# Kernel optimization log

Hardware: AMD Instinct MI355X
Metric: run time of the kernel (lower is better)

The kernel has to match this reference:

```python
import jax, jax.numpy as jnp
import numpy as np

NUM_CLASS = 5
IN_SIZE = 4
OBS_LEN = 20
EMBED = 256
B = 2048
N = 64
NUM_MODES = 20
IN_DIM = IN_SIZE * OBS_LEN  # 80


def setup_inputs() -> dict:
    key = jax.random.key(0)
    ks = jax.random.split(key, 12)
    s = 1.0 / np.sqrt(IN_DIM)
    inp = {
        "obs": jax.random.normal(ks[0], (B, OBS_LEN, IN_SIZE), jnp.float32),
        "neis": jax.random.normal(ks[1], (B, N, OBS_LEN, IN_SIZE), jnp.float32),
        "self_labels": jax.random.randint(ks[2], (B,), 0, NUM_CLASS),
        "nei_labels": jax.random.randint(ks[3], (B, N), 0, NUM_CLASS + 1),
        "modes": jax.random.normal(ks[4], (NUM_CLASS, NUM_MODES, EMBED), jnp.float32),
        # per-class obs embedding (ModuleList of Linear(in_dim, embed))
        "obs_W": jax.random.uniform(ks[5], (NUM_CLASS, IN_DIM, EMBED), jnp.float32, -s, s),
        "obs_b": jax.random.uniform(ks[6], (NUM_CLASS, EMBED), jnp.float32, -s, s),
        # per-class neighbor embedding (num_class+1 Linears)
        "nei_W": jax.random.uniform(ks[7], (NUM_CLASS + 1, IN_DIM, EMBED), jnp.float32, -s, s),
        "nei_b": jax.random.uniform(ks[8], (NUM_CLASS + 1, EMBED), jnp.float32, -s, s),
        # mode embedding Linear(2*embed, embed)
        "mode_W": jax.random.uniform(ks[9], (2 * EMBED, EMBED), jnp.float32, -1.0 / np.sqrt(2 * EMBED), 1.0 / np.sqrt(2 * EMBED)),
        "mode_b": jax.random.uniform(ks[10], (EMBED,), jnp.float32, -1.0 / np.sqrt(2 * EMBED), 1.0 / np.sqrt(2 * EMBED)),
    }
    return inp


def reference(obs, neis, self_labels, nei_labels, modes, obs_W, obs_b, nei_W, nei_b, mode_W, mode_b):
    obs_f = obs.reshape(B, IN_DIM)            # [B, in_dim]
    neis_f = neis.reshape(B, N, IN_DIM)       # [B, N, in_dim]
    eps = jnp.float32(1e-4)

    # label-routed obs embedding: one-hot selects the per-class Linear
    oh_s = jax.nn.one_hot(self_labels, NUM_CLASS, dtype=obs.dtype)          # [B, C]
    x = jnp.einsum("bi,cio,bc->bo", obs_f, obs_W, oh_s) + obs_b[self_labels]  # [B, E]

    # elementwise reciprocal transform (class-independent, applied to every neighbor row)
    r = jnp.where(neis_f >= 0, 1.0 / (neis_f + eps), 1.0 / (neis_f - eps))   # [B, N, in_dim]

    # label-routed neighbor embedding over num_class+1 experts
    oh_n = jax.nn.one_hot(nei_labels, NUM_CLASS + 1, dtype=obs.dtype)        # [B, N, C+1]
    nei_feats = jnp.einsum("bni,cio,bnc->bno", r, nei_W, oh_n) + nei_b[nei_labels]  # [B, N, E]

    mode_feats = modes[self_labels]                                          # [B, M, E]
    x_tiled = jnp.broadcast_to(x[:, None, :], (B, NUM_MODES, EMBED))
    cat = jnp.concatenate([x_tiled, mode_feats], axis=-1)                    # [B, M, 2E]
    out = jnp.einsum("bmk,ko->bmo", cat, mode_W) + mode_b                    # [B, M, E]
    return (out, nei_feats)
```

## Files before the change

kernel.cpp:

```cpp
#include <hip/hip_runtime.h>

#define BATCH 2048
#define NNEI 64
#define IN_DIM 80
#define EMBED 256
#define NCLS 5
#define NMODES 20
#define NROWS (BATCH * NNEI)
#define NEXP (NCLS + 1)
#define BPC2 256
#define TM 16

typedef __attribute__((ext_vector_type(8))) short bf16x8;
typedef __attribute__((ext_vector_type(4))) float f32x4;
typedef __attribute__((ext_vector_type(4))) int i32x4;

__device__ inline unsigned short bf16_rne(float f) {
    unsigned u = __builtin_bit_cast(unsigned, f);
    unsigned r = (u + 0x7fffu + ((u >> 16) & 1u)) >> 16;
    return (unsigned short)r;
}
__device__ inline float bf16_to_f(unsigned short h) {
    unsigned u = ((unsigned)h) << 16;
    return __builtin_bit_cast(float, u);
}

__global__ void count_labels(const int* __restrict__ nei_labels, int* __restrict__ counts) {
    __shared__ int lc[NEXP];
    int t = threadIdx.x;
    if (t < NEXP) lc[t] = 0;
    __syncthreads();
    atomicAdd(&lc[nei_labels[blockIdx.x * 256 + t]], 1);
    __syncthreads();
    if (t < NEXP) atomicAdd(&counts[t], lc[t]);
}

__global__ void scan_offsets(const int* __restrict__ counts,
                             int* __restrict__ offsets, int* __restrict__ cursors) {
    int s = 0;
    for (int c = 0; c < NEXP; ++c) { offsets[c] = s; cursors[c] = s; s += counts[c]; }
}

__global__ void place_rows(const int* __restrict__ nei_labels,
                           int* __restrict__ cursors, int* __restrict__ rowids) {
    __shared__ int lc[NEXP], lb[NEXP];
    int t = threadIdx.x;
    if (t < NEXP) lc[t] = 0;
    __syncthreads();
    int r = blockIdx.x * 256 + t;
    int c = nei_labels[r];
    int lpos = atomicAdd(&lc[c], 1);
    __syncthreads();
    if (t < NEXP) lb[t] = atomicAdd(&cursors[t], lc[t]);
    __syncthreads();
    rowids[lb[c] + lpos] = r;
}

__global__ void wfrag_prep(const float* __restrict__ nei_W, unsigned short* __restrict__ wfrag) {
    int e = blockIdx.x;
    int l = threadIdx.x;
    int part = e & 1;
    int cfg = (e >> 1) & 15;
    int ks = (e >> 5) % 3;
    int c = e / 96;
    int col = cfg * 16 + (l & 15);
    unsigned short v[8] __attribute__((aligned(16)));
    #pragma unroll
    for (int j = 0; j < 8; ++j) {
        int k = ks * 32 + ((l >> 4) * 8) + j;
        float w = (k < IN_DIM) ? nei_W[((size_t)c * IN_DIM + k) * EMBED + col] : 0.f;
        unsigned short h = bf16_rne(w);
        if (part == 0) v[j] = h;
        else v[j] = bf16_rne(w - bf16_to_f(h));
    }
    unsigned short* dst = wfrag + ((size_t)e * 64 + l) * 8;
    *reinterpret_cast<i32x4*>(dst) = *reinterpret_cast<const i32x4*>(v);
}

__global__ void mode_proj(const float* __restrict__ modes,
                          const float* __restrict__ mode_W,
                          const float* __restrict__ mode_b,
                          float* __restrict__ proj) {
    int cm = blockIdx.x;
    int o = threadIdx.x;
    const float* mv = modes + (size_t)cm * EMBED;
    float acc = mode_b[o];
    #pragma unroll 8
    for (int k = 0; k < EMBED; ++k)
        acc = fmaf(mv[k], mode_W[(size_t)(EMBED + k) * EMBED + o], acc);
    proj[(size_t)cm * EMBED + o] = acc;
}

#define BPB 4
__global__ __launch_bounds__(256, 2)
void obs_mode(const float* __restrict__ obs, const int* __restrict__ self_labels,
              const float* __restrict__ obs_W, const float* __restrict__ obs_b,
              const float* __restrict__ mode_W, const float* __restrict__ proj,
              float* __restrict__ out0) {
    int b0 = blockIdx.x * BPB;
    int o = threadIdx.x;
    __shared__ float obs_s[BPB][IN_DIM];
    __shared__ float x_s[BPB][EMBED];
    __shared__ int cls_s[BPB];

    for (int t = threadIdx.x; t < BPB * IN_DIM; t += 256) {
        int bb = t / IN_DIM, k = t % IN_DIM;
        obs_s[bb][k] = obs[(size_t)(b0 + bb) * IN_DIM + k];
    }
    if (threadIdx.x < BPB) cls_s[threadIdx.x] = self_labels[b0 + threadIdx.x];
    __syncthreads();

    int c[BPB];
    float xacc[BPB];
    #pragma unroll
    for (int bb = 0; bb < BPB; ++bb) {
        c[bb] = cls_s[bb];
        xacc[bb] = obs_b[c[bb] * EMBED + o];
    }
    #pragma unroll 8
    for (int k = 0; k < IN_DIM; ++k) {
        #pragma unroll
        for (int bb = 0; bb < BPB; ++bb)
            xacc[bb] = fmaf(obs_s[bb][k],
                            obs_W[(size_t)c[bb] * IN_DIM * EMBED + (size_t)k * EMBED + o],
                            xacc[bb]);
    }
    #pragma unroll
    for (int bb = 0; bb < BPB; ++bb) x_s[bb][o] = xacc[bb];
    __syncthreads();

    float tacc[BPB] = {0.f, 0.f, 0.f, 0.f};
    #pragma unroll 8
    for (int k = 0; k < EMBED; ++k) {
        float wv = mode_W[(size_t)k * EMBED + o];
        #pragma unroll
        for (int bb = 0; bb < BPB; ++bb)
            tacc[bb] = fmaf(x_s[bb][k], wv, tacc[bb]);
    }
    #pragma unroll
    for (int bb = 0; bb < BPB; ++bb) {
        const float* pj = proj + (size_t)c[bb] * NMODES * EMBED;
        float* op = out0 + (size_t)(b0 + bb) * NMODES * EMBED;
        for (int m = 0; m < NMODES; ++m)
            op[m * EMBED + o] = tacc[bb] + pj[m * EMBED + o];
    }
}

__global__ __launch_bounds__(256)
void nei_gemv_mfma(const float* __restrict__ neis,
                   const unsigned short* __restrict__ wfrag,
                   const float* __restrict__ nei_b,
                   const int* __restrict__ counts, const int* __restrict__ offsets,
                   const int* __restrict__ rowids,
                   float* __restrict__ out_n) {
    const int c = blockIdx.x / BPC2;
    const int blk = blockIdx.x % BPC2;
    const int cnt = counts[c];
    const int ntiles = (cnt + TM - 1) / TM;
    if (blk >= ntiles) return;

    const int ch = threadIdx.x >> 6;
    const int l = threadIdx.x & 63;
    const int* mylist = rowids + offsets[c];

    bf16x8 wh[3][4], wl[3][4];
    {
        const unsigned short* wb = wfrag + (size_t)c * 96 * 64 * 8;
        #pragma unroll
        for (int ks = 0; ks < 3; ++ks)
            #pragma unroll
            for (int cf = 0; cf < 4; ++cf) {
                size_t base = ((((size_t)ks * 16 + (ch * 4 + cf)) * 2) * 64 + l) * 8;
                wh[ks][cf] = *reinterpret_cast<const bf16x8*>(wb + base);
                wl[ks][cf] = *reinterpret_cast<const bf16x8*>(wb + base + 64 * 8);
            }
    }
    float bias[4];
    #pragma unroll
    for (int cf = 0; cf < 4; ++cf)
        bias[cf] = nei_b[c * EMBED + (ch * 4 + cf) * 16 + (l & 15)];

    const int kc = (l >> 4) * 8;

    for (int tile = blk; tile < ntiles; tile += BPC2) {
        int gi = tile * TM + (l & 15);
        int rid = mylist[min(gi, cnt - 1)];
        const float* base = neis + (size_t)rid * IN_DIM;

        float f[24];
        #pragma unroll
        for (int ks = 0; ks < 3; ++ks) {
            int k0 = ks * 32 + kc;
            if (k0 + 8 > IN_DIM) k0 = 0;
            float4 x0 = *reinterpret_cast<const float4*>(base + k0);
            float4 x1 = *reinterpret_cast<const float4*>(base + k0 + 4);
            f[ks * 8 + 0] = x0.x; f[ks * 8 + 1] = x0.y; f[ks * 8 + 2] = x0.z; f[ks * 8 + 3] = x0.w;
            f[ks * 8 + 4] = x1.x; f[ks * 8 + 5] = x1.y; f[ks * 8 + 6] = x1.z; f[ks * 8 + 7] = x1.w;
        }

        bf16x8 ah[3], al[3];
        #pragma unroll
        for (int ks = 0; ks < 3; ++ks) {
            #pragma unroll
            for (int j = 0; j < 8; ++j) {
                float v = f[ks * 8 + j];
                float d = (v >= 0.f) ? (v + 1e-4f) : (v - 1e-4f);
                float r = __builtin_amdgcn_rcpf(d);
                unsigned short hi = bf16_rne(r);
                ah[ks][j] = (short)hi;
                al[ks][j] = (short)bf16_rne(r - bf16_to_f(hi));
            }
        }

        f32x4 acc[4];
        #pragma unroll
        for (int cf = 0; cf < 4; ++cf) acc[cf] = (f32x4){0.f, 0.f, 0.f, 0.f};
        #pragma unroll
        for (int ks = 0; ks < 3; ++ks) {
            #pragma unroll
            for (int cf = 0; cf < 4; ++cf) {
                acc[cf] = __builtin_amdgcn_mfma_f32_16x16x32_bf16(ah[ks], wh[ks][cf], acc[cf], 0, 0, 0);
                acc[cf] = __builtin_amdgcn_mfma_f32_16x16x32_bf16(al[ks], wh[ks][cf], acc[cf], 0, 0, 0);
                acc[cf] = __builtin_amdgcn_mfma_f32_16x16x32_bf16(ah[ks], wl[ks][cf], acc[cf], 0, 0, 0);
            }
        }

        int rb = (l >> 4) * 4;
        #pragma unroll
        for (int i = 0; i < 4; ++i) {
            int rid_i = __shfl(rid, rb + i);
            if (tile * TM + rb + i < cnt) {
                float* op = out_n + (size_t)rid_i * EMBED + (l & 15);
                #pragma unroll
                for (int cf = 0; cf < 4; ++cf)
                    op[(ch * 4 + cf) * 16] = acc[cf][i] + bias[cf];
            }
        }
    }
}

extern "C" void kernel_launch(void* const* d_in, const int* in_sizes, int n_in,
                              void* d_out, int out_size, void* d_ws, size_t ws_size,
                              hipStream_t stream) {
    const float* obs         = (const float*)d_in[0];
    const float* neis        = (const float*)d_in[1];
    const int*   self_labels = (const int*)d_in[2];
    const int*   nei_labels  = (const int*)d_in[3];
    const float* modes       = (const float*)d_in[4];
    const float* obs_W       = (const float*)d_in[5];
    const float* obs_b       = (const float*)d_in[6];
    const float* nei_W       = (const float*)d_in[7];
    const float* nei_b       = (const float*)d_in[8];
    const float* mode_W      = (const float*)d_in[9];
    const float* mode_b      = (const float*)d_in[10];

    float* out0  = (float*)d_out;
    float* out_n = out0 + (size_t)BATCH * NMODES * EMBED;

    char* ws = (char*)d_ws;
    int* counts  = (int*)ws;
    int* offsets = (int*)(ws + 64);
    int* cursors = (int*)(ws + 128);
    int* rowids  = (int*)(ws + 256);
    float* proj  = (float*)(ws + 256 + (size_t)NROWS * 4);
    unsigned short* wfrag = (unsigned short*)(ws + 256 + (size_t)NROWS * 4
                                              + (size_t)NCLS * NMODES * EMBED * 4);

    hipMemsetAsync(counts, 0, NEXP * sizeof(int), stream);

    count_labels<<<NROWS / 256, 256, 0, stream>>>(nei_labels, counts);
    scan_offsets<<<1, 1, 0, stream>>>(counts, offsets, cursors);
    place_rows<<<NROWS / 256, 256, 0, stream>>>(nei_labels, cursors, rowids);
    wfrag_prep<<<NEXP * 96, 64, 0, stream>>>(nei_W, wfrag);
    mode_proj<<<NCLS * NMODES, 256, 0, stream>>>(modes, mode_W, mode_b, proj);
    obs_mode<<<BATCH / BPB, 256, 0, stream>>>(obs, self_labels, obs_W, obs_b,
                                              mode_W, proj, out0);
    nei_gemv_mfma<<<NEXP * BPC2, 256, 0, stream>>>(neis, wfrag, nei_b,
                                                   counts, offsets, rowids, out_n);
}
```

Measured before the change: 113.7 us.

## Merge label binning into one pass, shrink grid and double-buffer neighbor tile loads

The separate count, scan and place kernels become a single binning kernel that writes row ids into per-class fixed-stride lists, which removes two launches. The neighbor MFMA kernel now runs on a 512-block grid split across the classes, with launch bounds allowing 2 blocks per unit. Its tile loop is software-pipelined with two register buffers so the next tile's global loads overlap the current tile's MFMA work. obs_mode processes 8 batch rows per block instead of 4. The costs are a much larger workspace for the per-class lists, higher register pressure from the double buffers, and fewer blocks per class.

After: 111.0 us. -2.4%, faster.

```diff
diff --git a/kernel.cpp b/kernel.cpp
--- a/kernel.cpp
+++ b/kernel.cpp
@@ -8,8 +8,8 @@
 #define NMODES 20
 #define NROWS (BATCH * NNEI)
 #define NEXP (NCLS + 1)
-#define BPC2 256
 #define TM 16
+#define GRID2 512
 
 typedef __attribute__((ext_vector_type(8))) short bf16x8;
 typedef __attribute__((ext_vector_type(4))) float f32x4;
@@ -25,24 +25,8 @@
     return __builtin_bit_cast(float, u);
 }
 
-__global__ void count_labels(const int* __restrict__ nei_labels, int* __restrict__ counts) {
-    __shared__ int lc[NEXP];
-    int t = threadIdx.x;
-    if (t < NEXP) lc[t] = 0;
-    __syncthreads();
-    atomicAdd(&lc[nei_labels[blockIdx.x * 256 + t]], 1);
-    __syncthreads();
-    if (t < NEXP) atomicAdd(&counts[t], lc[t]);
-}
-
-__global__ void scan_offsets(const int* __restrict__ counts,
-                             int* __restrict__ offsets, int* __restrict__ cursors) {
-    int s = 0;
-    for (int c = 0; c < NEXP; ++c) { offsets[c] = s; cursors[c] = s; s += counts[c]; }
-}
-
-__global__ void place_rows(const int* __restrict__ nei_labels,
-                           int* __restrict__ cursors, int* __restrict__ rowids) {
+__global__ void bin_rows(const int* __restrict__ nei_labels,
+                         int* __restrict__ counts, int* __restrict__ lists) {
     __shared__ int lc[NEXP], lb[NEXP];
     int t = threadIdx.x;
     if (t < NEXP) lc[t] = 0;
@@ -51,9 +35,9 @@
     int c = nei_labels[r];
     int lpos = atomicAdd(&lc[c], 1);
     __syncthreads();
-    if (t < NEXP) lb[t] = atomicAdd(&cursors[t], lc[t]);
-    __syncthreads();
-    rowids[lb[c] + lpos] = r;
+    if (t < NEXP) lb[t] = atomicAdd(&counts[t], lc[t]);
+    __syncthreads();
+    lists[(size_t)c * NROWS + lb[c] + lpos] = r;
 }
 
 __global__ void wfrag_prep(const float* __restrict__ nei_W, unsigned short* __restrict__ wfrag) {
@@ -91,7 +75,7 @@
     proj[(size_t)cm * EMBED + o] = acc;
 }
 
-#define BPB 4
+#define BPB 8
 __global__ __launch_bounds__(256, 2)
 void obs_mode(const float* __restrict__ obs, const int* __restrict__ self_labels,
               const float* __restrict__ obs_W, const float* __restrict__ obs_b,
@@ -117,7 +101,7 @@
         c[bb] = cls_s[bb];
         xacc[bb] = obs_b[c[bb] * EMBED + o];
     }
-    #pragma unroll 8
+    #pragma unroll 4
     for (int k = 0; k < IN_DIM; ++k) {
         #pragma unroll
         for (int bb = 0; bb < BPB; ++bb)
@@ -129,8 +113,10 @@
     for (int bb = 0; bb < BPB; ++bb) x_s[bb][o] = xacc[bb];
     __syncthreads();
 
-    float tacc[BPB] = {0.f, 0.f, 0.f, 0.f};
-    #pragma unroll 8
+    float tacc[BPB];
+    #pragma unroll
+    for (int bb = 0; bb < BPB; ++bb) tacc[bb] = 0.f;
+    #pragma unroll 4
     for (int k = 0; k < EMBED; ++k) {
         float wv = mode_W[(size_t)k * EMBED + o];
         #pragma unroll
@@ -146,22 +132,27 @@
     }
 }
 
-__global__ __launch_bounds__(256)
+__global__ __launch_bounds__(256, 2)
 void nei_gemv_mfma(const float* __restrict__ neis,
                    const unsigned short* __restrict__ wfrag,
                    const float* __restrict__ nei_b,
-                   const int* __restrict__ counts, const int* __restrict__ offsets,
-                   const int* __restrict__ rowids,
+                   const int* __restrict__ counts,
+                   const int* __restrict__ lists,
                    float* __restrict__ out_n) {
-    const int c = blockIdx.x / BPC2;
-    const int blk = blockIdx.x % BPC2;
+    const int b = blockIdx.x;
+    const int c = (b * NEXP) / GRID2;
+    const int cstart = (c * GRID2 + NEXP - 1) / NEXP;
+    const int cend = ((c + 1) * GRID2 + NEXP - 1) / NEXP;
+    const int blk = b - cstart;
+    const int nblk = cend - cstart;
     const int cnt = counts[c];
     const int ntiles = (cnt + TM - 1) / TM;
-    if (blk >= ntiles) return;
+    if (blk >= ntiles || cnt == 0) return;
 
     const int ch = threadIdx.x >> 6;
     const int l = threadIdx.x & 63;
-    const int* mylist = rowids + offsets[c];
+    const int* mylist = lists + (size_t)c * NROWS;
+    const int kc = (l >> 4) * 8;
 
     bf16x8 wh[3][4], wl[3][4];
     {
@@ -180,63 +171,76 @@
     for (int cf = 0; cf < 4; ++cf)
         bias[cf] = nei_b[c * EMBED + (ch * 4 + cf) * 16 + (l & 15)];
 
-    const int kc = (l >> 4) * 8;
-
-    for (int tile = blk; tile < ntiles; tile += BPC2) {
-        int gi = tile * TM + (l & 15);
-        int rid = mylist[min(gi, cnt - 1)];
-        const float* base = neis + (size_t)rid * IN_DIM;
-
-        float f[24];
-        #pragma unroll
-        for (int ks = 0; ks < 3; ++ks) {
-            int k0 = ks * 32 + kc;
-            if (k0 + 8 > IN_DIM) k0 = 0;
-            float4 x0 = *reinterpret_cast<const float4*>(base + k0);
-            float4 x1 = *reinterpret_cast<const float4*>(base + k0 + 4);
-            f[ks * 8 + 0] = x0.x; f[ks * 8 + 1] = x0.y; f[ks * 8 + 2] = x0.z; f[ks * 8 + 3] = x0.w;
-            f[ks * 8 + 4] = x1.x; f[ks * 8 + 5] = x1.y; f[ks * 8 + 6] = x1.z; f[ks * 8 + 7] = x1.w;
-        }
-
-        bf16x8 ah[3], al[3];
-        #pragma unroll
-        for (int ks = 0; ks < 3; ++ks) {
-            #pragma unroll
-            for (int j = 0; j < 8; ++j) {
-                float v = f[ks * 8 + j];
-                float d = (v >= 0.f) ? (v + 1e-4f) : (v - 1e-4f);
-                float r = __builtin_amdgcn_rcpf(d);
-                unsigned short hi = bf16_rne(r);
-                ah[ks][j] = (short)hi;
-                al[ks][j] = (short)bf16_rne(r - bf16_to_f(hi));
-            }
-        }
-
-        f32x4 acc[4];
-        #pragma unroll
-        for (int cf = 0; cf < 4; ++cf) acc[cf] = (f32x4){0.f, 0.f, 0.f, 0.f};
-        #pragma unroll
-        for (int ks = 0; ks < 3; ++ks) {
-            #pragma unroll
-            for (int cf = 0; cf < 4; ++cf) {
-                acc[cf] = __builtin_amdgcn_mfma_f32_16x16x32_bf16(ah[ks], wh[ks][cf], acc[cf], 0, 0, 0);
-                acc[cf] = __builtin_amdgcn_mfma_f32_16x16x32_bf16(al[ks], wh[ks][cf], acc[cf], 0, 0, 0);
-                acc[cf] = __builtin_amdgcn_mfma_f32_16x16x32_bf16(ah[ks], wl[ks][cf], acc[cf], 0, 0, 0);
-            }
-        }
-
-        int rb = (l >> 4) * 4;
-        #pragma unroll
-        for (int i = 0; i < 4; ++i) {
-            int rid_i = __shfl(rid, rb + i);
-            if (tile * TM + rb + i < cnt) {
-                float* op = out_n + (size_t)rid_i * EMBED + (l & 15);
-                #pragma unroll
-                for (int cf = 0; cf < 4; ++cf)
-                    op[(ch * 4 + cf) * 16] = acc[cf][i] + bias[cf];
-            }
-        }
-    }
+#define LOADT(F, R, T) {                                                      \
+    int gi_ = (T) * TM + (l & 15);                                            \
+    R = mylist[min(gi_, cnt - 1)];                                            \
+    const float* bp_ = neis + (size_t)(unsigned)R * IN_DIM;                   \
+    _Pragma("unroll")                                                         \
+    for (int ks_ = 0; ks_ < 3; ++ks_) {                                       \
+        int k0_ = ks_ * 32 + kc;                                              \
+        if (k0_ + 8 > IN_DIM) k0_ = 0;          \
+        *reinterpret_cast<float4*>(&F[ks_ * 8])     = *reinterpret_cast<const float4*>(bp_ + k0_);     \
+        *reinterpret_cast<float4*>(&F[ks_ * 8 + 4]) = *reinterpret_cast<const float4*>(bp_ + k0_ + 4); \
+    } }
+
+#define COMPT(F, R, T) {                                                      \
+    bf16x8 ah_[3], al_[3];                                                    \
+    _Pragma("unroll")                                                         \
+    for (int ks_ = 0; ks_ < 3; ++ks_) {                                       \
+        _Pragma("unroll")                                                     \
+        for (int j_ = 0; j_ < 8; ++j_) {                                      \
+            float v_ = F[ks_ * 8 + j_];                                       \
+            float d_ = (v_ >= 0.f) ? (v_ + 1e-4f) : (v_ - 1e-4f);             \
+            float r_ = __builtin_amdgcn_rcpf(d_);                             \
+            unsigned short hi_ = bf16_rne(r_);                                \
+            ah_[ks_][j_] = (short)hi_;                                        \
+            al_[ks_][j_] = (short)bf16_rne(r_ - bf16_to_f(hi_));              \
+        }                                                                     \
+    }                                                                         \
+    f32x4 acc_[4];                                                            \
+    _Pragma("unroll")                                                         \
+    for (int cf_ = 0; cf_ < 4; ++cf_) acc_[cf_] = (f32x4){0.f, 0.f, 0.f, 0.f};\
+    _Pragma("unroll")                                                         \
+    for (int ks_ = 0; ks_ < 3; ++ks_) {                                       \
+        _Pragma("unroll")                                                     \
+        for (int cf_ = 0; cf_ < 4; ++cf_) {                                   \
+            acc_[cf_] = __builtin_amdgcn_mfma_f32_16x16x32_bf16(ah_[ks_], wh[ks_][cf_], acc_[cf_], 0, 0, 0); \
+            acc_[cf_] = __builtin_amdgcn_mfma_f32_16x16x32_bf16(al_[ks_], wh[ks_][cf_], acc_[cf_], 0, 0, 0); \
+            acc_[cf_] = __builtin_amdgcn_mfma_f32_16x16x32_bf16(ah_[ks_], wl[ks_][cf_], acc_[cf_], 0, 0, 0); \
+        }                                                                     \
+    }                                                                         \
+    int rb_ = (l >> 4) * 4;                                                   \
+    _Pragma("unroll")                                                         \
+    for (int i_ = 0; i_ < 4; ++i_) {                                          \
+        int rid_ = __shfl(R, rb_ + i_);                                       \
+        if ((T) * TM + rb_ + i_ < cnt) {                                      \
+            float* op_ = out_n + (size_t)(unsigned)rid_ * EMBED + (l & 15);   \
+            _Pragma("unroll")                                                 \
+            for (int cf_ = 0; cf_ < 4; ++cf_)                                 \
+                op_[(ch * 4 + cf_) * 16] = acc_[cf_][i_] + bias[cf_];         \
+        }                                                                     \
+    } }
+
+    float fA[24], fB[24];
+    int ridA, ridB;
+    int tile = blk;
+    LOADT(fA, ridA, tile)
+    while (true) {
+        int nt = tile + nblk;
+        bool hn = nt < ntiles;
+        if (hn) LOADT(fB, ridB, nt)
+        COMPT(fA, ridA, tile)
+        if (!hn) break;
+        tile = nt;
+        nt = tile + nblk;
+        hn = nt < ntiles;
+        if (hn) LOADT(fA, ridA, nt)
+        COMPT(fB, ridB, tile)
+        if (!hn) break;
+        tile = nt;
+    }
+#undef LOADT
+#undef COMPT
 }
 
 extern "C" void kernel_launch(void* const* d_in, const int* in_sizes, int n_in,
@@ -258,23 +262,19 @@
     float* out_n = out0 + (size_t)BATCH * NMODES * EMBED;
 
     char* ws = (char*)d_ws;
-    int* counts  = (int*)ws;
-    int* offsets = (int*)(ws + 64);
-    int* cursors = (int*)(ws + 128);
-    int* rowids  = (int*)(ws + 256);
-    float* proj  = (float*)(ws + 256 + (size_t)NROWS * 4);
-    unsigned short* wfrag = (unsigned short*)(ws + 256 + (size_t)NROWS * 4
+    int* counts = (int*)ws;
+    int* lists  = (int*)(ws + 256);
+    float* proj = (float*)(ws + 256 + (size_t)NEXP * NROWS * 4);
+    unsigned short* wfrag = (unsigned short*)(ws + 256 + (size_t)NEXP * NROWS * 4
                                               + (size_t)NCLS * NMODES * EMBED * 4);
 
     hipMemsetAsync(counts, 0, NEXP * sizeof(int), stream);
 
-    count_labels<<<NROWS / 256, 256, 0, stream>>>(nei_labels, counts);
-    scan_offsets<<<1, 1, 0, stream>>>(counts, offsets, cursors);
-    place_rows<<<NROWS / 256, 256, 0, stream>>>(nei_labels, cursors, rowids);
+    bin_rows<<<NROWS / 256, 256, 0, stream>>>(nei_labels, counts, lists);
     wfrag_prep<<<NEXP * 96, 64, 0, stream>>>(nei_W, wfrag);
     mode_proj<<<NCLS * NMODES, 256, 0, stream>>>(modes, mode_W, mode_b, proj);
     obs_mode<<<BATCH / BPB, 256, 0, stream>>>(obs, self_labels, obs_W, obs_b,
                                               mode_W, proj, out0);
-    nei_gemv_mfma<<<NEXP * BPC2, 256, 0, stream>>>(neis, wfrag, nei_b,
-                                                   counts, offsets, rowids, out_n);
-}
+    nei_gemv_mfma<<<GRID2, 256, 0, stream>>>(neis, wfrag, nei_b,
+                                             counts, lists, out_n);
+}
```

## Pre-pack reciprocal bf16 tiles and stage neighbor outputs through LDS

Applied to the files above, without the earlier changes.

Replaces the count/scan/place sequence with a single per-class binning pass that writes into fixed per-class lists. A new pack_tiles kernel does the reciprocal transform and the hi/lo bf16 split once, and lays the result out in MFMA fragment order in a workspace buffer. The GEMM kernel then loads those fragments directly and writes its output through a double-buffered LDS tile, so each row is stored as coalesced float4 rows. Separately, obs_mode now processes 8 batch rows per block. The cost is an extra kernel and a round trip through global memory for the packed tiles, in exchange for less scattered gather and store traffic.

After: 130.1 us. 1.14x slower.

```diff
diff --git a/kernel.cpp b/kernel.cpp
--- a/kernel.cpp
+++ b/kernel.cpp
@@ -8,12 +8,15 @@
 #define NMODES 20
 #define NROWS (BATCH * NNEI)
 #define NEXP (NCLS + 1)
-#define BPC2 256
 #define TM 16
+#define NTILES_MAX 8208
+#define GRIDB 768
+#define TILE_SH 3072
 
 typedef __attribute__((ext_vector_type(8))) short bf16x8;
 typedef __attribute__((ext_vector_type(4))) float f32x4;
 typedef __attribute__((ext_vector_type(4))) int i32x4;
+typedef __attribute__((ext_vector_type(2))) int i32x2;
 
 __device__ inline unsigned short bf16_rne(float f) {
     unsigned u = __builtin_bit_cast(unsigned, f);
@@ -25,24 +28,8 @@
     return __builtin_bit_cast(float, u);
 }
 
-__global__ void count_labels(const int* __restrict__ nei_labels, int* __restrict__ counts) {
-    __shared__ int lc[NEXP];
-    int t = threadIdx.x;
-    if (t < NEXP) lc[t] = 0;
-    __syncthreads();
-    atomicAdd(&lc[nei_labels[blockIdx.x * 256 + t]], 1);
-    __syncthreads();
-    if (t < NEXP) atomicAdd(&counts[t], lc[t]);
-}
-
-__global__ void scan_offsets(const int* __restrict__ counts,
-                             int* __restrict__ offsets, int* __restrict__ cursors) {
-    int s = 0;
-    for (int c = 0; c < NEXP; ++c) { offsets[c] = s; cursors[c] = s; s += counts[c]; }
-}
-
-__global__ void place_rows(const int* __restrict__ nei_labels,
-                           int* __restrict__ cursors, int* __restrict__ rowids) {
+__global__ void bin_rows(const int* __restrict__ nei_labels,
+                         int* __restrict__ counts, int* __restrict__ lists) {
     __shared__ int lc[NEXP], lb[NEXP];
     int t = threadIdx.x;
     if (t < NEXP) lc[t] = 0;
@@ -51,9 +38,64 @@
     int c = nei_labels[r];
     int lpos = atomicAdd(&lc[c], 1);
     __syncthreads();
-    if (t < NEXP) lb[t] = atomicAdd(&cursors[t], lc[t]);
-    __syncthreads();
-    rowids[lb[c] + lpos] = r;
+    if (t < NEXP) lb[t] = atomicAdd(&counts[t], lc[t]);
+    __syncthreads();
+    lists[(size_t)c * NROWS + lb[c] + lpos] = r;
+}
+
+__global__ void scan_tiles(const int* __restrict__ counts, int* __restrict__ tileoff) {
+    int s = 0;
+    for (int c = 0; c < NEXP; ++c) { tileoff[c] = s; s += (counts[c] + TM - 1) / TM; }
+    tileoff[NEXP] = s;
+}
+
+__global__ void pack_tiles(const float* __restrict__ neis,
+                           const int* __restrict__ counts, const int* __restrict__ tileoff,
+                           const int* __restrict__ lists,
+                           unsigned short* __restrict__ packbuf) {
+    int bt = blockIdx.x;
+    int c = -1;
+    #pragma unroll
+    for (int i = 0; i < NEXP; ++i)
+        if (bt >= tileoff[i] && bt < tileoff[i + 1]) c = i;
+    if (c < 0) return;
+    int lt = bt - tileoff[c];
+    int cnt = counts[c];
+    const int* mylist = lists + (size_t)c * NROWS;
+    unsigned short* tb = packbuf + (size_t)bt * TILE_SH;
+    int t = threadIdx.x;
+
+    if (t < 64) {
+        int part = t >> 5, lane = 32 + (t & 31);
+        *reinterpret_cast<i32x4*>(tb + 2 * 1024 + part * 512 + lane * 8) = (i32x4){0, 0, 0, 0};
+    }
+
+    for (int f = t; f < 320; f += 256) {
+        int row = f / 20, q = f - row * 20;
+        int gi = lt * TM + row;
+        int ks = q >> 3, lg = (q >> 1) & 3, half = q & 1;
+        unsigned short* dhi = tb + ks * 1024 + (row + (lg << 4)) * 8 + half * 4;
+        unsigned short hv[4] __attribute__((aligned(8)));
+        unsigned short lv[4] __attribute__((aligned(8)));
+        if (gi < cnt) {
+            int rid = mylist[gi];
+            float4 v = *reinterpret_cast<const float4*>(neis + (size_t)rid * IN_DIM + q * 4);
+            float vv[4] = {v.x, v.y, v.z, v.w};
+            #pragma unroll
+            for (int j = 0; j < 4; ++j) {
+                float d = (vv[j] >= 0.f) ? (vv[j] + 1e-4f) : (vv[j] - 1e-4f);
+                float r = __builtin_amdgcn_rcpf(d);
+                unsigned short hi = bf16_rne(r);
+                hv[j] = hi;
+                lv[j] = bf16_rne(r - bf16_to_f(hi));
+            }
+        } else {
+            #pragma unroll
+            for (int j = 0; j < 4; ++j) { hv[j] = 0; lv[j] = 0; }
+        }
+        *reinterpret_cast<i32x2*>(dhi)       = *reinterpret_cast<const i32x2*>(hv);
+        *reinterpret_cast<i32x2*>(dhi + 512) = *reinterpret_cast<const i32x2*>(lv);
+    }
 }
 
 __global__ void wfrag_prep(const float* __restrict__ nei_W, unsigned short* __restrict__ wfrag) {
@@ -91,7 +133,7 @@
     proj[(size_t)cm * EMBED + o] = acc;
 }
 
-#define BPB 4
+#define BPB 8
 __global__ __launch_bounds__(256, 2)
 void obs_mode(const float* __restrict__ obs, const int* __restrict__ self_labels,
               const float* __restrict__ obs_W, const float* __restrict__ obs_b,
@@ -117,7 +159,7 @@
         c[bb] = cls_s[bb];
         xacc[bb] = obs_b[c[bb] * EMBED + o];
     }
-    #pragma unroll 8
+    #pragma unroll 4
     for (int k = 0; k < IN_DIM; ++k) {
         #pragma unroll
         for (int bb = 0; bb < BPB; ++bb)
@@ -129,8 +171,10 @@
     for (int bb = 0; bb < BPB; ++bb) x_s[bb][o] = xacc[bb];
     __syncthreads();
 
-    float tacc[BPB] = {0.f, 0.f, 0.f, 0.f};
-    #pragma unroll 8
+    float tacc[BPB];
+    #pragma unroll
+    for (int bb = 0; bb < BPB; ++bb) tacc[bb] = 0.f;
+    #pragma unroll 4
     for (int k = 0; k < EMBED; ++k) {
         float wv = mode_W[(size_t)k * EMBED + o];
         #pragma unroll
@@ -146,22 +190,26 @@
     }
 }
 
-__global__ __launch_bounds__(256)
-void nei_gemv_mfma(const float* __restrict__ neis,
-                   const unsigned short* __restrict__ wfrag,
-                   const float* __restrict__ nei_b,
-                   const int* __restrict__ counts, const int* __restrict__ offsets,
-                   const int* __restrict__ rowids,
-                   float* __restrict__ out_n) {
-    const int c = blockIdx.x / BPC2;
-    const int blk = blockIdx.x % BPC2;
+__global__ __launch_bounds__(256, 3)
+void nei_gemm2(const unsigned short* __restrict__ packbuf,
+               const unsigned short* __restrict__ wfrag,
+               const float* __restrict__ nei_b,
+               const int* __restrict__ counts, const int* __restrict__ tileoff,
+               const int* __restrict__ lists,
+               float* __restrict__ out_n) {
+    const int b = blockIdx.x;
+    const int c = b / (GRIDB / NEXP);
+    const int blk = b - c * (GRIDB / NEXP);
+    const int nblk = GRIDB / NEXP;
     const int cnt = counts[c];
-    const int ntiles = (cnt + TM - 1) / TM;
+    const int to_c = tileoff[c];
+    const int ntiles = tileoff[c + 1] - to_c;
     if (blk >= ntiles) return;
 
-    const int ch = threadIdx.x >> 6;
-    const int l = threadIdx.x & 63;
-    const int* mylist = rowids + offsets[c];
+    const int t = threadIdx.x;
+    const int ch = t >> 6;
+    const int l = t & 63;
+    const int* mylist = lists + (size_t)c * NROWS;
 
     bf16x8 wh[3][4], wl[3][4];
     {
@@ -180,38 +228,22 @@
     for (int cf = 0; cf < 4; ++cf)
         bias[cf] = nei_b[c * EMBED + (ch * 4 + cf) * 16 + (l & 15)];
 
-    const int kc = (l >> 4) * 8;
-
-    for (int tile = blk; tile < ntiles; tile += BPC2) {
-        int gi = tile * TM + (l & 15);
-        int rid = mylist[min(gi, cnt - 1)];
-        const float* base = neis + (size_t)rid * IN_DIM;
-
-        float f[24];
+    __shared__ float buf[2][TM][EMBED + 4];
+    __shared__ int rid_s[2][TM];
+
+    int cur = 0;
+    for (int lt = blk; lt < ntiles; lt += nblk) {
+        const unsigned short* tb = packbuf + (size_t)(to_c + lt) * TILE_SH;
+        if (t < TM) {
+            int gi = lt * TM + t;
+            rid_s[cur][t] = (gi < cnt) ? mylist[gi] : -1;
+        }
+        bf16x8 ah[3], al[3];
         #pragma unroll
         for (int ks = 0; ks < 3; ++ks) {
-            int k0 = ks * 32 + kc;
-            if (k0 + 8 > IN_DIM) k0 = 0;
-            float4 x0 = *reinterpret_cast<const float4*>(base + k0);
-            float4 x1 = *reinterpret_cast<const float4*>(base + k0 + 4);
-            f[ks * 8 + 0] = x0.x; f[ks * 8 + 1] = x0.y; f[ks * 8 + 2] = x0.z; f[ks * 8 + 3] = x0.w;
-            f[ks * 8 + 4] = x1.x; f[ks * 8 + 5] = x1.y; f[ks * 8 + 6] = x1.z; f[ks * 8 + 7] = x1.w;
-        }
-
-        bf16x8 ah[3], al[3];
-        #pragma unroll
-        for (int ks = 0; ks < 3; ++ks) {
-            #pragma unroll
-            for (int j = 0; j < 8; ++j) {
-                float v = f[ks * 8 + j];
-                float d = (v >= 0.f) ? (v + 1e-4f) : (v - 1e-4f);
-                float r = __builtin_amdgcn_rcpf(d);
-                unsigned short hi = bf16_rne(r);
-                ah[ks][j] = (short)hi;
-                al[ks][j] = (short)bf16_rne(r - bf16_to_f(hi));
-            }
-        }
-
+            ah[ks] = *reinterpret_cast<const bf16x8*>(tb + ks * 1024 + l * 8);
+            al[ks] = *reinterpret_cast<const bf16x8*>(tb + ks * 1024 + 512 + l * 8);
+        }
         f32x4 acc[4];
         #pragma unroll
         for (int cf = 0; cf < 4; ++cf) acc[cf] = (f32x4){0.f, 0.f, 0.f, 0.f};
@@ -224,18 +256,28 @@
                 acc[cf] = __builtin_amdgcn_mfma_f32_16x16x32_bf16(ah[ks], wl[ks][cf], acc[cf], 0, 0, 0);
             }
         }
-
-        int rb = (l >> 4) * 4;
-        #pragma unroll
-        for (int i = 0; i < 4; ++i) {
-            int rid_i = __shfl(rid, rb + i);
-            if (tile * TM + rb + i < cnt) {
-                float* op = out_n + (size_t)rid_i * EMBED + (l & 15);
+        #pragma unroll
+        for (int cf = 0; cf < 4; ++cf) {
+            int col = ch * 64 + cf * 16 + (l & 15);
+            #pragma unroll
+            for (int i = 0; i < 4; ++i)
+                buf[cur][(l >> 4) * 4 + i][col] = acc[cf][i] + bias[cf];
+        }
+        __syncthreads();
+        {
+            int row = t >> 4, seg = t & 15;
+            int rid = rid_s[cur][row];
+            if (rid >= 0) {
+                float* op = out_n + (size_t)rid * EMBED;
                 #pragma unroll
-                for (int cf = 0; cf < 4; ++cf)
-                    op[(ch * 4 + cf) * 16] = acc[cf][i] + bias[cf];
+                for (int sb = 0; sb < 4; ++sb) {
+                    int s4 = (seg + sb * 16) * 4;
+                    float4 vv = *reinterpret_cast<const float4*>(&buf[cur][row][s4]);
+                    *reinterpret_cast<float4*>(op + s4) = vv;
+                }
             }
         }
+        cur ^= 1;
     }
 }
 
@@ -259,22 +301,24 @@
 
     char* ws = (char*)d_ws;
     int* counts  = (int*)ws;
-    int* offsets = (int*)(ws + 64);
-    int* cursors = (int*)(ws + 128);
-    int* rowids  = (int*)(ws + 256);
-    float* proj  = (float*)(ws + 256 + (size_t)NROWS * 4);
-    unsigned short* wfrag = (unsigned short*)(ws + 256 + (size_t)NROWS * 4
-                                              + (size_t)NCLS * NMODES * EMBED * 4);
+    int* tileoff = (int*)(ws + 64);
+    int* lists   = (int*)(ws + 256);
+    size_t off = 256 + (size_t)NEXP * NROWS * 4;
+    float* proj = (float*)(ws + off);
+    off += (size_t)NCLS * NMODES * EMBED * 4;
+    unsigned short* wfrag = (unsigned short*)(ws + off);
+    off += (size_t)NEXP * 96 * 64 * 8 * 2;
+    unsigned short* packbuf = (unsigned short*)(ws + off);
 
     hipMemsetAsync(counts, 0, NEXP * sizeof(int), stream);
 
-    count_labels<<<NROWS / 256, 256, 0, stream>>>(nei_labels, counts);
-    scan_offsets<<<1, 1, 0, stream>>>(counts, offsets, cursors);
-    place_rows<<<NROWS / 256, 256, 0, stream>>>(nei_labels, cursors, rowids);
+    bin_rows<<<NROWS / 256, 256, 0, stream>>>(nei_labels, counts, lists);
+    scan_tiles<<<1, 1, 0, stream>>>(counts, tileoff);
+    pack_tiles<<<NTILES_MAX, 256, 0, stream>>>(neis, counts, tileoff, lists, packbuf);
     wfrag_prep<<<NEXP * 96, 64, 0, stream>>>(nei_W, wfrag);
     mode_proj<<<NCLS * NMODES, 256, 0, stream>>>(modes, mode_W, mode_b, proj);
     obs_mode<<<BATCH / BPB, 256, 0, stream>>>(obs, self_labels, obs_W, obs_b,
                                               mode_W, proj, out0);
-    nei_gemv_mfma<<<NEXP * BPC2, 256, 0, stream>>>(neis, wfrag, nei_b,
-                                                   counts, offsets, rowids, out_n);
-}
+    nei_gemm2<<<GRIDB, 256, 0, stream>>>(packbuf, wfrag, nei_b,
+                                         counts, tileoff, lists, out_n);
+}
```
